# Kernel tuning notes

Measured on AMD Instinct MI355X. Metric: run time of the kernel, lower is better.

The kernel has to match this reference:

```python
import jax, jax.numpy as jnp
import numpy as np

CH = 256
CR = 8  # channel_reduce


def conv1x1(x, w, b):
    # x: [b,c,h,w], w: [o,c], b: [o]
    return jnp.einsum('oc,bchw->bohw', w, x) + b[None, :, None, None]


def maxpool2(x):
    b, c, h, w = x.shape
    return x.reshape(b, c, h // 2, 2, w // 2, 2).max(axis=(3, 5))


def setup_inputs() -> dict:
    key = jax.random.key(0)
    ks = jax.random.split(key, 10)
    ch = CH
    cr = ch // CR      # 32
    c2 = ch // 2       # 128
    s = 0.05
    return {
        'x': jax.random.normal(ks[0], (8, ch, 64, 64), jnp.float32),
        'w_theta': jax.random.normal(ks[1], (cr, ch), jnp.float32) * s,
        'b_theta': jnp.zeros((cr,), jnp.float32),
        'w_phi': jax.random.normal(ks[2], (cr, ch), jnp.float32) * s,
        'b_phi': jnp.zeros((cr,), jnp.float32),
        'w_g': jax.random.normal(ks[3], (c2, ch), jnp.float32) * s,
        'b_g': jnp.zeros((c2,), jnp.float32),
        'w_last': jax.random.normal(ks[4], (ch, c2), jnp.float32) * s,
        'b_last': jnp.zeros((ch,), jnp.float32),
        'gamma': jnp.zeros((1,), jnp.float32),
    }


def reference(x, w_theta, b_theta, w_phi, b_phi, w_g, b_g, w_last, b_last, gamma):
    bs, ch, wi, hi = x.shape
    L = wi * hi
    L4 = L // 4
    # theta: [bs, ch//8, L] -> [bs, L, ch//8]
    theta = conv1x1(x, w_theta, b_theta).reshape(bs, ch // 8, L).transpose(0, 2, 1)
    # phi: 1x1 conv, maxpool 2 -> [bs, ch//8, L//4]
    phi = maxpool2(conv1x1(x, w_phi, b_phi)).reshape(bs, ch // 8, L4)
    energy = jnp.einsum('bld,bdm->blm', theta, phi)  # [bs, L, L4]
    # Faithful to F.softmax(energy) with no dim on a 3D tensor: torch uses dim=0
    attn = jax.nn.softmax(energy, axis=0)
    # g: 1x1 conv, maxpool 2 -> memory layout [bs, ch//2, L4], then the original
    # reinterprets (view) it as [bs, L4, ch//2] without transposing — replicate.
    g = maxpool2(conv1x1(x, w_g, b_g)).reshape(bs, L4, ch // 2)
    attn_g = jnp.einsum('blm,bmc->blc', attn, g)  # [bs, L, ch//2]
    # Original views [bs, L, ch//2] as [bs, ch//2, wi, hi] — again a raw reshape.
    attn_g = attn_g.reshape(bs, ch // 2, wi, hi)
    attn_g = conv1x1(attn_g, w_last, b_last)
    out = gamma[0] * attn_g + x
    return (out, attn)
```

## Files before the change

kernel.cpp:

```cpp
#include <hip/hip_runtime.h>
#include <math.h>

#define BATCH 8
#define CH    256
#define D     32
#define C2    128
#define LTOT  4096
#define MTOT  1024

#define TH_OFF  0u
#define PHI_OFF 1048576u
#define G_OFF   1310720u
#define AG_OFF  2359296u
#define OUT_ELEMS 8388608u

__global__ __launch_bounds__(256)
void prep_kernel(const float* __restrict__ x,
                 const float* __restrict__ w_theta, const float* __restrict__ b_theta,
                 const float* __restrict__ w_phi,   const float* __restrict__ b_phi,
                 const float* __restrict__ gamma,
                 float* __restrict__ theta_ws, float* __restrict__ phi_ws,
                 float* __restrict__ out)
{
    __shared__ float xs[32][132];
    __shared__ float wT[32][68];

    const int t  = threadIdx.x;
    const int b  = blockIdx.x >> 5;
    const int lt = blockIdx.x & 31;
    const int l0 = lt * 128;
    const float g0 = gamma[0];

    const int dg = t >> 4;
    const int lg = t & 15;

    float acc[4][8];
#pragma unroll
    for (int i = 0; i < 4; ++i)
#pragma unroll
        for (int j = 0; j < 8; ++j) acc[i][j] = 0.f;

    const int rr = t >> 3;
    const int rc = (t & 7) * 16;
    const int wd = t >> 2;
    const int wc = (t & 3) * 8;

    for (int cc = 0; cc < 8; ++cc) {
        {
            const size_t goff = ((size_t)(b * CH + cc * 32 + rr)) * LTOT + l0 + rc;
            const float* src = x + goff;
            float4 v0 = *(const float4*)(src);
            float4 v1 = *(const float4*)(src + 4);
            float4 v2 = *(const float4*)(src + 8);
            float4 v3 = *(const float4*)(src + 12);
            *(float4*)&xs[rr][rc]      = v0;
            *(float4*)&xs[rr][rc + 4]  = v1;
            *(float4*)&xs[rr][rc + 8]  = v2;
            *(float4*)&xs[rr][rc + 12] = v3;
            if (g0 == 0.0f) {
                float* odst = out + goff;
                *(float4*)(odst)      = v0;
                *(float4*)(odst + 4)  = v1;
                *(float4*)(odst + 8)  = v2;
                *(float4*)(odst + 12) = v3;
            }
        }
        {
            const float* wsrc = (wd < 32 ? (w_theta + wd * CH)
                                         : (w_phi + (wd - 32) * CH)) + cc * 32 + wc;
            float4 w0 = *(const float4*)(wsrc);
            float4 w1 = *(const float4*)(wsrc + 4);
            wT[wc + 0][wd] = w0.x; wT[wc + 1][wd] = w0.y;
            wT[wc + 2][wd] = w0.z; wT[wc + 3][wd] = w0.w;
            wT[wc + 4][wd] = w1.x; wT[wc + 5][wd] = w1.y;
            wT[wc + 6][wd] = w1.z; wT[wc + 7][wd] = w1.w;
        }
        __syncthreads();
#pragma unroll
        for (int c = 0; c < 32; ++c) {
            float4 a4 = *(const float4*)&wT[c][dg * 4];
            float4 x0 = *(const float4*)&xs[c][lg * 8];
            float4 x1 = *(const float4*)&xs[c][lg * 8 + 4];
            const float av[4] = {a4.x, a4.y, a4.z, a4.w};
            const float xv[8] = {x0.x, x0.y, x0.z, x0.w, x1.x, x1.y, x1.z, x1.w};
#pragma unroll
            for (int i = 0; i < 4; ++i)
#pragma unroll
                for (int j = 0; j < 8; ++j)
                    acc[i][j] = fmaf(av[i], xv[j], acc[i][j]);
        }
        __syncthreads();
    }

    if (dg < 8) {
#pragma unroll
        for (int i = 0; i < 4; ++i) {
            const int d = dg * 4 + i;
            const float bias = b_theta[d];
            float* dst = theta_ws + ((size_t)(b * D + d)) * LTOT + l0 + lg * 8;
            float4 o0 = {acc[i][0] + bias, acc[i][1] + bias, acc[i][2] + bias, acc[i][3] + bias};
            float4 o1 = {acc[i][4] + bias, acc[i][5] + bias, acc[i][6] + bias, acc[i][7] + bias};
            *(float4*)dst       = o0;
            *(float4*)(dst + 4) = o1;
        }
    } else {
#pragma unroll
        for (int i = 0; i < 4; ++i) {
            const int d = dg * 4 + i - 32;
#pragma unroll
            for (int j = 0; j < 8; ++j) xs[d][lg * 8 + j] = acc[i][j];
        }
    }
    __syncthreads();
    {
        const int d  = t >> 3;
        const int m4 = (t & 7) * 4;
        const float bias = b_phi[d];
        float4 r;
#pragma unroll
        for (int j = 0; j < 4; ++j) {
            const int ml = m4 + j;
            float v = fmaxf(fmaxf(xs[d][2 * ml], xs[d][2 * ml + 1]),
                            fmaxf(xs[d][64 + 2 * ml], xs[d][64 + 2 * ml + 1]));
            ((float*)&r)[j] = v + bias;
        }
        *(float4*)(phi_ws + ((size_t)(b * D + d)) * MTOT + lt * 32 + m4) = r;
    }
}

__global__ __launch_bounds__(256)
void attn_kernel(const float* __restrict__ theta_ws,
                 const float* __restrict__ phi_ws,
                 float* __restrict__ attn_out)
{
    __shared__ float th[8 * 516];
    __shared__ float ph[8 * 1028];

    const int t  = threadIdx.x;
    const int lt = blockIdx.x;
    const int mt = blockIdx.y;
    const int l0 = lt * 16;
    const int m0 = mt * 32;

    {
        const int sb = t >> 5, sd = t & 31;
        const float* tsrc = theta_ws + ((size_t)(sb * D + sd)) * LTOT + l0;
        float* tdst = &th[sb * 516 + sd * 16];
#pragma unroll
        for (int q = 0; q < 4; ++q)
            *(float4*)(tdst + q * 4) = *(const float4*)(tsrc + q * 4);
        const float* psrc = phi_ws + ((size_t)(sb * D + sd)) * MTOT + m0;
        float* pdst = &ph[sb * 1028 + sd * 32];
#pragma unroll
        for (int q = 0; q < 8; ++q)
            *(float4*)(pdst + q * 4) = *(const float4*)(psrc + q * 4);
    }
    __syncthreads();

    const int lane = t & 63;
    const int wv   = t >> 6;
    const int b    = lane & 7;
    const int s    = lane >> 3;

    const float* tp = &th[b * 516 + wv * 4];
    const float* pp = &ph[b * 1028 + s * 4];

    float acc[4][4];
#pragma unroll
    for (int i = 0; i < 4; ++i)
#pragma unroll
        for (int j = 0; j < 4; ++j) acc[i][j] = 0.f;

#pragma unroll
    for (int d = 0; d < 32; ++d) {
        float4 t4 = *(const float4*)(tp + d * 16);
        float4 p4 = *(const float4*)(pp + d * 32);
        const float tv[4] = {t4.x, t4.y, t4.z, t4.w};
        const float pv[4] = {p4.x, p4.y, p4.z, p4.w};
#pragma unroll
        for (int i = 0; i < 4; ++i)
#pragma unroll
            for (int j = 0; j < 4; ++j)
                acc[i][j] = fmaf(tv[i], pv[j], acc[i][j]);
    }

    float o[4][4];
#pragma unroll
    for (int i = 0; i < 4; ++i) {
#pragma unroll
        for (int j = 0; j < 4; ++j) {
            float e  = acc[i][j];
            float mx = e;
            mx = fmaxf(mx, __shfl_xor(mx, 1));
            mx = fmaxf(mx, __shfl_xor(mx, 2));
            mx = fmaxf(mx, __shfl_xor(mx, 4));
            float ex = __expf(e - mx);
            float sm = ex;
            sm += __shfl_xor(sm, 1);
            sm += __shfl_xor(sm, 2);
            sm += __shfl_xor(sm, 4);
            o[i][j] = ex * __builtin_amdgcn_rcpf(sm);
        }
    }

#pragma unroll
    for (int i = 0; i < 4; ++i) {
        float4 w = {o[i][0], o[i][1], o[i][2], o[i][3]};
        *(float4*)(attn_out + ((size_t)b << 22)
                   + (size_t)(l0 + wv * 4 + i) * MTOT + m0 + s * 4) = w;
    }
}

__global__ void g_kernel(const float* __restrict__ x, const float* __restrict__ w_g,
                         const float* __restrict__ b_g, const float* __restrict__ gamma,
                         float* __restrict__ g_ws)
{
    if (gamma[0] == 0.0f) return;
    const int idx = blockIdx.x * 256 + threadIdx.x;
    const int m  = idx & 1023;
    const int c2 = (idx >> 10) & 127;
    const int b  = idx >> 17;
    const int mh = m >> 5, mw = m & 31;
    const int base_l = mh * 128 + mw * 2;
    float s0 = b_g[c2], s1 = s0, s2 = s0, s3 = s0;
    const float* xb = x + (size_t)b * CH * LTOT;
    const float* wr = w_g + c2 * CH;
    for (int c = 0; c < CH; ++c) {
        const float* xc = xb + c * LTOT + base_l;
        const float w = wr[c];
        s0 = fmaf(w, xc[0],  s0);
        s1 = fmaf(w, xc[1],  s1);
        s2 = fmaf(w, xc[64], s2);
        s3 = fmaf(w, xc[65], s3);
    }
    g_ws[idx] = fmaxf(fmaxf(s0, s1), fmaxf(s2, s3));
}

__global__ void ag_kernel(const float* __restrict__ attn, const float* __restrict__ g_ws,
                          const float* __restrict__ gamma, float* __restrict__ ag_ws)
{
    if (gamma[0] == 0.0f) return;
    const int idx = blockIdx.x * 256 + threadIdx.x;
    const int c = idx & 127;
    const int l = (idx >> 7) & 4095;
    const int b = idx >> 19;
    const float* ar = attn + ((size_t)b << 22) + (size_t)l * MTOT;
    const float* gb = g_ws + (size_t)b * (C2 * MTOT);
    float s = 0.f;
    for (int m = 0; m < MTOT; ++m)
        s = fmaf(ar[m], gb[m * C2 + c], s);
    ag_ws[idx] = s;
}

__global__ void last_kernel(const float* __restrict__ x, const float* __restrict__ w_last,
                            const float* __restrict__ b_last, const float* __restrict__ gamma,
                            const float* __restrict__ ag_ws, float* __restrict__ out)
{
    const float g0 = gamma[0];
    if (g0 == 0.0f) return;
    const int idx = blockIdx.x * 256 + threadIdx.x;
    const int l = idx & 4095;
    const int o = (idx >> 12) & 255;
    const int b = idx >> 20;
    const float* agb = ag_ws + (size_t)b * (C2 * LTOT);
    float s = b_last[o];
    for (int c2 = 0; c2 < C2; ++c2)
        s = fmaf(w_last[o * C2 + c2], agb[c2 * LTOT + l], s);
    out[idx] = g0 * s + x[idx];
}

extern "C" void kernel_launch(void* const* d_in, const int* in_sizes, int n_in,
                              void* d_out, int out_size, void* d_ws, size_t ws_size,
                              hipStream_t stream)
{
    const float* x       = (const float*)d_in[0];
    const float* w_theta = (const float*)d_in[1];
    const float* b_theta = (const float*)d_in[2];
    const float* w_phi   = (const float*)d_in[3];
    const float* b_phi   = (const float*)d_in[4];
    const float* w_g     = (const float*)d_in[5];
    const float* b_g     = (const float*)d_in[6];
    const float* w_last  = (const float*)d_in[7];
    const float* b_last  = (const float*)d_in[8];
    const float* gamma   = (const float*)d_in[9];

    float* out  = (float*)d_out;
    float* attn = out + OUT_ELEMS;
    float* ws   = (float*)d_ws;
    float* theta_ws = ws + TH_OFF;
    float* phi_ws   = ws + PHI_OFF;
    float* g_ws     = ws + G_OFF;
    float* ag_ws    = ws + AG_OFF;

    prep_kernel<<<256, 256, 0, stream>>>(x, w_theta, b_theta, w_phi, b_phi,
                                         gamma, theta_ws, phi_ws, out);
    attn_kernel<<<dim3(256, 32), 256, 0, stream>>>(theta_ws, phi_ws, attn);
    g_kernel<<<4096, 256, 0, stream>>>(x, w_g, b_g, gamma, g_ws);
    ag_kernel<<<16384, 256, 0, stream>>>(attn, g_ws, gamma, ag_ws);
    last_kernel<<<32768, 256, 0, stream>>>(x, w_last, b_last, gamma, ag_ws, out);
}
```

Measured before the change: 312.2 us.

## Retile attention kernel, split prep by projection, grid-stride skipped kernels

The prep kernel now uses twice as many blocks, each computing either the theta or the phi projection, which halves per-block work and register use. The attention kernel computes a 16x4 tile per thread, reading theta straight from global memory instead of staging it in shared memory. It also drops the max-subtraction in the batch-axis softmax, which is only safe when energies stay small. The g, ag and last kernels become grid-stride loops with much smaller grids, so far fewer blocks launch only to exit early when gamma is zero.

```diff
diff --git a/kernel.cpp b/kernel.cpp
--- a/kernel.cpp
+++ b/kernel.cpp
@@ -23,27 +23,31 @@
                  float* __restrict__ out)
 {
     __shared__ float xs[32][132];
-    __shared__ float wT[32][68];
+    __shared__ float wT[32][36];
 
     const int t  = threadIdx.x;
-    const int b  = blockIdx.x >> 5;
-    const int lt = blockIdx.x & 31;
+    const int tt = blockIdx.x & 1;
+    const int lt = (blockIdx.x >> 1) & 31;
+    const int b  = blockIdx.x >> 6;
     const int l0 = lt * 128;
     const float g0 = gamma[0];
 
     const int dg = t >> 4;
     const int lg = t & 15;
 
-    float acc[4][8];
-#pragma unroll
-    for (int i = 0; i < 4; ++i)
+    float acc[2][8];
+#pragma unroll
+    for (int i = 0; i < 2; ++i)
 #pragma unroll
         for (int j = 0; j < 8; ++j) acc[i][j] = 0.f;
 
     const int rr = t >> 3;
     const int rc = (t & 7) * 16;
-    const int wd = t >> 2;
-    const int wc = (t & 3) * 8;
+    const int wd = t >> 3;
+    const int wc = (t & 7) * 4;
+
+    const float* wmat = tt ? w_phi : w_theta;
+    const bool do_copy = (tt == 0) && (g0 == 0.0f);
 
     for (int cc = 0; cc < 8; ++cc) {
         {
@@ -57,7 +61,7 @@
             *(float4*)&xs[rr][rc + 4]  = v1;
             *(float4*)&xs[rr][rc + 8]  = v2;
             *(float4*)&xs[rr][rc + 12] = v3;
-            if (g0 == 0.0f) {
+            if (do_copy) {
                 float* odst = out + goff;
                 *(float4*)(odst)      = v0;
                 *(float4*)(odst + 4)  = v1;
@@ -66,36 +70,30 @@
             }
         }
         {
-            const float* wsrc = (wd < 32 ? (w_theta + wd * CH)
-                                         : (w_phi + (wd - 32) * CH)) + cc * 32 + wc;
-            float4 w0 = *(const float4*)(wsrc);
-            float4 w1 = *(const float4*)(wsrc + 4);
+            float4 w0 = *(const float4*)(wmat + wd * CH + cc * 32 + wc);
             wT[wc + 0][wd] = w0.x; wT[wc + 1][wd] = w0.y;
             wT[wc + 2][wd] = w0.z; wT[wc + 3][wd] = w0.w;
-            wT[wc + 4][wd] = w1.x; wT[wc + 5][wd] = w1.y;
-            wT[wc + 6][wd] = w1.z; wT[wc + 7][wd] = w1.w;
         }
         __syncthreads();
 #pragma unroll
         for (int c = 0; c < 32; ++c) {
-            float4 a4 = *(const float4*)&wT[c][dg * 4];
+            float2 a2 = *(const float2*)&wT[c][dg * 2];
             float4 x0 = *(const float4*)&xs[c][lg * 8];
             float4 x1 = *(const float4*)&xs[c][lg * 8 + 4];
-            const float av[4] = {a4.x, a4.y, a4.z, a4.w};
             const float xv[8] = {x0.x, x0.y, x0.z, x0.w, x1.x, x1.y, x1.z, x1.w};
 #pragma unroll
-            for (int i = 0; i < 4; ++i)
-#pragma unroll
-                for (int j = 0; j < 8; ++j)
-                    acc[i][j] = fmaf(av[i], xv[j], acc[i][j]);
+            for (int j = 0; j < 8; ++j) {
+                acc[0][j] = fmaf(a2.x, xv[j], acc[0][j]);
+                acc[1][j] = fmaf(a2.y, xv[j], acc[1][j]);
+            }
         }
         __syncthreads();
     }
 
-    if (dg < 8) {
-#pragma unroll
-        for (int i = 0; i < 4; ++i) {
-            const int d = dg * 4 + i;
+    if (tt == 0) {
+#pragma unroll
+        for (int i = 0; i < 2; ++i) {
+            const int d = dg * 2 + i;
             const float bias = b_theta[d];
             float* dst = theta_ws + ((size_t)(b * D + d)) * LTOT + l0 + lg * 8;
             float4 o0 = {acc[i][0] + bias, acc[i][1] + bias, acc[i][2] + bias, acc[i][3] + bias};
@@ -105,14 +103,10 @@
         }
     } else {
 #pragma unroll
-        for (int i = 0; i < 4; ++i) {
-            const int d = dg * 4 + i - 32;
-#pragma unroll
-            for (int j = 0; j < 8; ++j) xs[d][lg * 8 + j] = acc[i][j];
-        }
-    }
-    __syncthreads();
-    {
+        for (int i = 0; i < 2; ++i)
+#pragma unroll
+            for (int j = 0; j < 8; ++j) xs[dg * 2 + i][lg * 8 + j] = acc[i][j];
+        __syncthreads();
         const int d  = t >> 3;
         const int m4 = (t & 7) * 4;
         const float bias = b_phi[d];
@@ -133,24 +127,16 @@
                  const float* __restrict__ phi_ws,
                  float* __restrict__ attn_out)
 {
-    __shared__ float th[8 * 516];
-    __shared__ float ph[8 * 1028];
+    __shared__ float ph[8 * 1156];
 
     const int t  = threadIdx.x;
-    const int lt = blockIdx.x;
-    const int mt = blockIdx.y;
-    const int l0 = lt * 16;
-    const int m0 = mt * 32;
+    const int l0 = blockIdx.x * 64;
+    const int m0 = blockIdx.y * 32;
 
     {
         const int sb = t >> 5, sd = t & 31;
-        const float* tsrc = theta_ws + ((size_t)(sb * D + sd)) * LTOT + l0;
-        float* tdst = &th[sb * 516 + sd * 16];
-#pragma unroll
-        for (int q = 0; q < 4; ++q)
-            *(float4*)(tdst + q * 4) = *(const float4*)(tsrc + q * 4);
         const float* psrc = phi_ws + ((size_t)(sb * D + sd)) * MTOT + m0;
-        float* pdst = &ph[sb * 1028 + sd * 32];
+        float* pdst = &ph[sb * 1156 + sd * 36];
 #pragma unroll
         for (int q = 0; q < 8; ++q)
             *(float4*)(pdst + q * 4) = *(const float4*)(psrc + q * 4);
@@ -162,52 +148,48 @@
     const int b    = lane & 7;
     const int s    = lane >> 3;
 
-    const float* tp = &th[b * 516 + wv * 4];
-    const float* pp = &ph[b * 1028 + s * 4];
-
-    float acc[4][4];
-#pragma unroll
-    for (int i = 0; i < 4; ++i)
+    const float* thp = theta_ws + ((size_t)(b * D)) * LTOT + l0 + wv * 16;
+    const float* pp  = &ph[b * 1156 + s * 4];
+
+    float acc[16][4];
+#pragma unroll
+    for (int i = 0; i < 16; ++i)
 #pragma unroll
         for (int j = 0; j < 4; ++j) acc[i][j] = 0.f;
 
-#pragma unroll
+#pragma unroll 2
     for (int d = 0; d < 32; ++d) {
-        float4 t4 = *(const float4*)(tp + d * 16);
-        float4 p4 = *(const float4*)(pp + d * 32);
-        const float tv[4] = {t4.x, t4.y, t4.z, t4.w};
+        float4 p4 = *(const float4*)(pp + d * 36);
+        const float* tq = thp + ((size_t)d) * LTOT;
+        float4 t0 = *(const float4*)(tq);
+        float4 t1 = *(const float4*)(tq + 4);
+        float4 t2 = *(const float4*)(tq + 8);
+        float4 t3 = *(const float4*)(tq + 12);
+        const float tv[16] = {t0.x, t0.y, t0.z, t0.w, t1.x, t1.y, t1.z, t1.w,
+                              t2.x, t2.y, t2.z, t2.w, t3.x, t3.y, t3.z, t3.w};
         const float pv[4] = {p4.x, p4.y, p4.z, p4.w};
 #pragma unroll
-        for (int i = 0; i < 4; ++i)
+        for (int i = 0; i < 16; ++i)
 #pragma unroll
             for (int j = 0; j < 4; ++j)
                 acc[i][j] = fmaf(tv[i], pv[j], acc[i][j]);
     }
 
-    float o[4][4];
-#pragma unroll
-    for (int i = 0; i < 4; ++i) {
+#pragma unroll
+    for (int i = 0; i < 16; ++i) {
+        float o[4];
 #pragma unroll
         for (int j = 0; j < 4; ++j) {
-            float e  = acc[i][j];
-            float mx = e;
-            mx = fmaxf(mx, __shfl_xor(mx, 1));
-            mx = fmaxf(mx, __shfl_xor(mx, 2));
-            mx = fmaxf(mx, __shfl_xor(mx, 4));
-            float ex = __expf(e - mx);
+            float ex = __expf(acc[i][j]);
             float sm = ex;
             sm += __shfl_xor(sm, 1);
             sm += __shfl_xor(sm, 2);
             sm += __shfl_xor(sm, 4);
-            o[i][j] = ex * __builtin_amdgcn_rcpf(sm);
-        }
-    }
-
-#pragma unroll
-    for (int i = 0; i < 4; ++i) {
-        float4 w = {o[i][0], o[i][1], o[i][2], o[i][3]};
+            o[j] = ex * __builtin_amdgcn_rcpf(sm);
+        }
+        float4 w = {o[0], o[1], o[2], o[3]};
         *(float4*)(attn_out + ((size_t)b << 22)
-                   + (size_t)(l0 + wv * 4 + i) * MTOT + m0 + s * 4) = w;
+                   + (size_t)(l0 + wv * 16 + i) * MTOT + m0 + s * 4) = w;
     }
 }
 
@@ -216,40 +198,44 @@
                          float* __restrict__ g_ws)
 {
     if (gamma[0] == 0.0f) return;
-    const int idx = blockIdx.x * 256 + threadIdx.x;
-    const int m  = idx & 1023;
-    const int c2 = (idx >> 10) & 127;
-    const int b  = idx >> 17;
-    const int mh = m >> 5, mw = m & 31;
-    const int base_l = mh * 128 + mw * 2;
-    float s0 = b_g[c2], s1 = s0, s2 = s0, s3 = s0;
-    const float* xb = x + (size_t)b * CH * LTOT;
-    const float* wr = w_g + c2 * CH;
-    for (int c = 0; c < CH; ++c) {
-        const float* xc = xb + c * LTOT + base_l;
-        const float w = wr[c];
-        s0 = fmaf(w, xc[0],  s0);
-        s1 = fmaf(w, xc[1],  s1);
-        s2 = fmaf(w, xc[64], s2);
-        s3 = fmaf(w, xc[65], s3);
-    }
-    g_ws[idx] = fmaxf(fmaxf(s0, s1), fmaxf(s2, s3));
+    const int N = BATCH * C2 * MTOT;
+    for (int idx = blockIdx.x * 256 + threadIdx.x; idx < N; idx += gridDim.x * 256) {
+        const int m  = idx & 1023;
+        const int c2 = (idx >> 10) & 127;
+        const int b  = idx >> 17;
+        const int mh = m >> 5, mw = m & 31;
+        const int base_l = mh * 128 + mw * 2;
+        float s0 = b_g[c2], s1 = s0, s2 = s0, s3 = s0;
+        const float* xb = x + (size_t)b * CH * LTOT;
+        const float* wr = w_g + c2 * CH;
+        for (int c = 0; c < CH; ++c) {
+            const float* xc = xb + c * LTOT + base_l;
+            const float w = wr[c];
+            s0 = fmaf(w, xc[0],  s0);
+            s1 = fmaf(w, xc[1],  s1);
+            s2 = fmaf(w, xc[64], s2);
+            s3 = fmaf(w, xc[65], s3);
+        }
+        g_ws[idx] = fmaxf(fmaxf(s0, s1), fmaxf(s2, s3));
+    }
 }
 
 __global__ void ag_kernel(const float* __restrict__ attn, const float* __restrict__ g_ws,
                           const float* __restrict__ gamma, float* __restrict__ ag_ws)
 {
     if (gamma[0] == 0.0f) return;
-    const int idx = blockIdx.x * 256 + threadIdx.x;
-    const int c = idx & 127;
-    const int l = (idx >> 7) & 4095;
-    const int b = idx >> 19;
-    const float* ar = attn + ((size_t)b << 22) + (size_t)l * MTOT;
-    const float* gb = g_ws + (size_t)b * (C2 * MTOT);
-    float s = 0.f;
-    for (int m = 0; m < MTOT; ++m)
-        s = fmaf(ar[m], gb[m * C2 + c], s);
-    ag_ws[idx] = s;
+    const int N = BATCH * LTOT * C2;
+    for (int idx = blockIdx.x * 256 + threadIdx.x; idx < N; idx += gridDim.x * 256) {
+        const int c = idx & 127;
+        const int l = (idx >> 7) & 4095;
+        const int b = idx >> 19;
+        const float* ar = attn + ((size_t)b << 22) + (size_t)l * MTOT;
+        const float* gb = g_ws + (size_t)b * (C2 * MTOT);
+        float s = 0.f;
+        for (int m = 0; m < MTOT; ++m)
+            s = fmaf(ar[m], gb[m * C2 + c], s);
+        ag_ws[idx] = s;
+    }
 }
 
 __global__ void last_kernel(const float* __restrict__ x, const float* __restrict__ w_last,
@@ -258,15 +244,17 @@
 {
     const float g0 = gamma[0];
     if (g0 == 0.0f) return;
-    const int idx = blockIdx.x * 256 + threadIdx.x;
-    const int l = idx & 4095;
-    const int o = (idx >> 12) & 255;
-    const int b = idx >> 20;
-    const float* agb = ag_ws + (size_t)b * (C2 * LTOT);
-    float s = b_last[o];
-    for (int c2 = 0; c2 < C2; ++c2)
-        s = fmaf(w_last[o * C2 + c2], agb[c2 * LTOT + l], s);
-    out[idx] = g0 * s + x[idx];
+    const int N = BATCH * CH * LTOT;
+    for (int idx = blockIdx.x * 256 + threadIdx.x; idx < N; idx += gridDim.x * 256) {
+        const int l = idx & 4095;
+        const int o = (idx >> 12) & 255;
+        const int b = idx >> 20;
+        const float* agb = ag_ws + (size_t)b * (C2 * LTOT);
+        float s = b_last[o];
+        for (int c2 = 0; c2 < C2; ++c2)
+            s = fmaf(w_last[o * C2 + c2], agb[c2 * LTOT + l], s);
+        out[idx] = g0 * s + x[idx];
+    }
 }
 
 extern "C" void kernel_launch(void* const* d_in, const int* in_sizes, int n_in,
@@ -292,10 +280,10 @@
     float* g_ws     = ws + G_OFF;
     float* ag_ws    = ws + AG_OFF;
 
-    prep_kernel<<<256, 256, 0, stream>>>(x, w_theta, b_theta, w_phi, b_phi,
+    prep_kernel<<<512, 256, 0, stream>>>(x, w_theta, b_theta, w_phi, b_phi,
                                          gamma, theta_ws, phi_ws, out);
-    attn_kernel<<<dim3(256, 32), 256, 0, stream>>>(theta_ws, phi_ws, attn);
-    g_kernel<<<4096, 256, 0, stream>>>(x, w_g, b_g, gamma, g_ws);
-    ag_kernel<<<16384, 256, 0, stream>>>(attn, g_ws, gamma, ag_ws);
-    last_kernel<<<32768, 256, 0, stream>>>(x, w_last, b_last, gamma, ag_ws, out);
-}
+    attn_kernel<<<dim3(64, 32), 256, 0, stream>>>(theta_ws, phi_ws, attn);
+    g_kernel<<<1024, 256, 0, stream>>>(x, w_g, b_g, gamma, g_ws);
+    ag_kernel<<<2048, 256, 0, stream>>>(attn, g_ws, gamma, ag_ws);
+    last_kernel<<<2048, 256, 0, stream>>>(x, w_last, b_last, gamma, ag_ws, out);
+}
```

Result: slower. 332.7 us (+6.6%).
